# Kernel optimization log

Hardware: AMD Instinct MI355X
Metric: run time of the kernel (lower is better)

## Reference

```python
import jax, jax.numpy as jnp
import numpy as np

NUM_FIELDS = 40
EMBED_DIM = 64
BATCH = 4096


def setup_inputs() -> dict:
    key = jax.random.key(0)
    k1, k2 = jax.random.split(key)
    x = jax.random.normal(k1, (BATCH, NUM_FIELDS, EMBED_DIM), dtype=jnp.float32)
    feat_embedding = jax.random.normal(k2, (NUM_FIELDS, NUM_FIELDS, EMBED_DIM), dtype=jnp.float32)
    return {"x": x, "feat_embedding": feat_embedding}


def reference(x, feat_embedding):
    # x: [B, F, E]; feat_embedding: [F, F, E]
    F = feat_embedding.shape[0]
    ii, jj = jnp.triu_indices(F, k=1)  # pair order matches the original i<j double loop
    # inter[p] = feat_embedding[i, j] * feat_embedding[j, i]  -> [P, E]
    inter = feat_embedding[ii, jj, :] * feat_embedding[jj, ii, :]
    # pairwise field products: [B, P, E]
    pair = x[:, ii, :] * x[:, jj, :]
    out = pair * inter[None, :, :]
    B = x.shape[0]
    return out.reshape(B, -1)  # concat along last dim in pair order
```

## Files before the change

kernel.cpp:

```cpp
#include <hip/hip_runtime.h>


#define NF 40
#define NE 64
#define NP 780
#define NPG 195

__global__ __launch_bounds__(256) void ffm_kernel(
    const float* __restrict__ x,
    const float* __restrict__ fe,
    float* __restrict__ out)
{
    __shared__ float xs[NF * NE];
    __shared__ int   pij[NP];

    const int tid = threadIdx.x;
    const int b   = blockIdx.x;

    if (tid < NF - 1) {
        const int i = tid;
        const int base = i * (2 * NF - i - 1) / 2;
        for (int j = i + 1; j < NF; ++j)
            pij[base + (j - i - 1)] = (i << 8) | j;
    }

    const float4* xb4 = (const float4*)(x + (size_t)b * (NF * NE));
    float4* xs4 = (float4*)xs;
    for (int idx = tid; idx < NF * NE / 4; idx += 256) xs4[idx] = xb4[idx];

    __syncthreads();

    const int wave = tid >> 6;
    const int lane = tid & 63;
    const int e4   = lane & 15;
    const int psub = lane >> 4;

    const float4* fe4 = (const float4*)fe;
    float4* ob4 = (float4*)(out + (size_t)b * (size_t)(NP * NE));

    for (int g = wave; g < NPG; g += 4) {
        const int p = g * 4 + psub;
        const int packed = pij[p];
        const int i = packed >> 8;
        const int j = packed & 255;

        const float4 xi  = xs4[i * 16 + e4];
        const float4 xj  = xs4[j * 16 + e4];
        const float4 fij = fe4[(i * NF + j) * 16 + e4];
        const float4 fji = fe4[(j * NF + i) * 16 + e4];

        float4 r;
        r.x = xi.x * xj.x * fij.x * fji.x;
        r.y = xi.y * xj.y * fij.y * fji.y;
        r.z = xi.z * xj.z * fij.z * fji.z;
        r.w = xi.w * xj.w * fij.w * fji.w;

        ob4[p * 16 + e4] = r;
    }
}

extern "C" void kernel_launch(void* const* d_in, const int* in_sizes, int n_in,
                              void* d_out, int out_size, void* d_ws, size_t ws_size,
                              hipStream_t stream) {
    const float* x  = (const float*)d_in[0];
    const float* fe = (const float*)d_in[1];
    float* out = (float*)d_out;

    const int B = in_sizes[0] / (NF * NE);
    ffm_kernel<<<dim3(B), dim3(256), 0, stream>>>(x, fe, out);
}
```

Before: 851.8 us.

## Precompute pairwise embedding products in a prekernel and use nontemporal stores

Adds a small prekernel that computes fe[i,j]*fe[j,i] once per pair and writes it, together with the pair index table, into workspace. The main kernel then reads one contiguous inter vector per pair instead of two strided fe gathers, and it stores the output with nontemporal hints. The aim is to cut redundant L2 gather traffic and multiplies, and to keep the large output write stream from polluting the cache. The cost is an extra kernel launch. The old fused kernel stays as a fallback when the workspace is too small.

```diff
diff --git a/kernel.cpp b/kernel.cpp
--- a/kernel.cpp
+++ b/kernel.cpp
@@ -1,12 +1,91 @@
 #include <hip/hip_runtime.h>
 
 
-#define NF 40
-#define NE 64
-#define NP 780
+#define NF  40
+#define NE  64
+#define NP  780
+#define NE4 16
 #define NPG 195
 
-__global__ __launch_bounds__(256) void ffm_kernel(
+typedef float f4v __attribute__((ext_vector_type(4)));
+
+__global__ __launch_bounds__(256) void ffm_pre(
+    const float* __restrict__ fe,
+    float* __restrict__ inter,
+    int* __restrict__ pij)
+{
+    const int idx = blockIdx.x * 256 + threadIdx.x;
+    if (idx >= NP * NE4) return;
+    const int p  = idx >> 4;
+    const int e4 = idx & 15;
+
+    int i = 0, base = 0;
+    while (p >= base + (NF - 1 - i)) { base += NF - 1 - i; ++i; }
+    const int j = i + 1 + (p - base);
+
+    if (e4 == 0) pij[p] = (i << 8) | j;
+
+    const float4 fij = ((const float4*)fe)[(i * NF + j) * NE4 + e4];
+    const float4 fji = ((const float4*)fe)[(j * NF + i) * NE4 + e4];
+    float4 r;
+    r.x = fij.x * fji.x;
+    r.y = fij.y * fji.y;
+    r.z = fij.z * fji.z;
+    r.w = fij.w * fji.w;
+    ((float4*)inter)[idx] = r;
+}
+
+__global__ __launch_bounds__(256) void ffm_main(
+    const float* __restrict__ x,
+    const float* __restrict__ inter,
+    const int* __restrict__ pij_g,
+    float* __restrict__ out)
+{
+    __shared__ float xs[NF * NE];
+    __shared__ int   pij[NP];
+
+    const int tid = threadIdx.x;
+    const int b   = blockIdx.x;
+
+    for (int idx = tid; idx < NP; idx += 256) pij[idx] = pij_g[idx];
+
+    const float4* xb4 = (const float4*)(x + (size_t)b * (NF * NE));
+    float4* xs4 = (float4*)xs;
+    for (int idx = tid; idx < NF * NE / 4; idx += 256) xs4[idx] = xb4[idx];
+
+    __syncthreads();
+
+    const int lane = tid & 63;
+    const int wave = tid >> 6;
+    const int e4   = lane & 15;
+
+    const f4v* in4 = (const f4v*)inter;
+    f4v* ob4 = (f4v*)out + (size_t)b * (size_t)(NP * NE4);
+    const float4* xs4c = (const float4*)xs;
+
+    int o = wave * 64 + lane;
+    #pragma unroll 2
+    for (int g = wave; g < NPG; g += 4, o += 256) {
+        const int p  = o >> 4;
+        const int pk = pij[p];
+        const int i  = pk >> 8;
+        const int j  = pk & 255;
+
+        const float4 xi = xs4c[(i << 4) + e4];
+        const float4 xj = xs4c[(j << 4) + e4];
+        const f4v    iv = in4[o];
+
+        f4v r;
+        r.x = (xi.x * xj.x) * iv.x;
+        r.y = (xi.y * xj.y) * iv.y;
+        r.z = (xi.z * xj.z) * iv.z;
+        r.w = (xi.w * xj.w) * iv.w;
+
+        __builtin_nontemporal_store(r, ob4 + o);
+    }
+}
+
+__global__ __launch_bounds__(256) void ffm_kernel_fb(
     const float* __restrict__ x,
     const float* __restrict__ fe,
     float* __restrict__ out)
@@ -50,10 +129,10 @@
         const float4 fji = fe4[(j * NF + i) * 16 + e4];
 
         float4 r;
-        r.x = xi.x * xj.x * fij.x * fji.x;
-        r.y = xi.y * xj.y * fij.y * fji.y;
-        r.z = xi.z * xj.z * fij.z * fji.z;
-        r.w = xi.w * xj.w * fij.w * fji.w;
+        r.x = (xi.x * xj.x) * (fij.x * fji.x);
+        r.y = (xi.y * xj.y) * (fij.y * fji.y);
+        r.z = (xi.z * xj.z) * (fij.z * fji.z);
+        r.w = (xi.w * xj.w) * (fij.w * fji.w);
 
         ob4[p * 16 + e4] = r;
     }
@@ -67,5 +146,18 @@
     float* out = (float*)d_out;
 
     const int B = in_sizes[0] / (NF * NE);
-    ffm_kernel<<<dim3(B), dim3(256), 0, stream>>>(x, fe, out);
+
+    const size_t inter_bytes = (size_t)NP * NE * sizeof(float);
+    const size_t pij_bytes   = (size_t)NP * sizeof(int);
+
+    if (ws_size >= inter_bytes + pij_bytes) {
+        float* inter = (float*)d_ws;
+        int*   pij   = (int*)((char*)d_ws + inter_bytes);
+
+        const int pre_blocks = (NP * NE4 + 255) / 256;
+        ffm_pre<<<dim3(pre_blocks), dim3(256), 0, stream>>>(fe, inter, pij);
+        ffm_main<<<dim3(B), dim3(256), 0, stream>>>(x, inter, pij, out);
+    } else {
+        ffm_kernel_fb<<<dim3(B), dim3(256), 0, stream>>>(x, fe, out);
+    }
 }
```

Measured after the change: 826.5 us. -3.0%, faster.
